# Kernel optimization log

Measured on AMD Instinct MI355X. Metric: run time of the kernel, lower is better.

Reference implementation:

```python
import jax, jax.numpy as jnp
import numpy as np

N = 4096            # total nodes in batched graph
B = 64              # number of graphs
NPG = 64            # nodes per graph (N = B * NPG)
HID = 64            # hidden_dim
INIT_EMB = 32       # init_emb_dim
POS = 32            # inp_dim (positional/structural feat)
KG = 100000         # num_nodes in KG embedding table
LAYER = 3           # num_gcn_layers


def setup_inputs() -> dict:
    key = jax.random.key(0)
    ks = jax.random.split(key, 10)
    # block-diagonal symmetric binary adjacency (batched graph, no self loops)
    gi = jnp.repeat(jnp.arange(B), NPG)                      # graph_indices [N]
    block = gi[:, None] == gi[None, :]
    u = jax.random.uniform(ks[0], (N, N)) < 0.1
    a = jnp.logical_and(jnp.logical_or(u, u.T), block)
    a = a.at[jnp.arange(N), jnp.arange(N)].set(False)
    adj = a.astype(jnp.float32)
    head_ids = jnp.arange(B) * NPG           # node with ndata['id']==1 per graph
    tail_ids = jnp.arange(B) * NPG + 1       # node with ndata['id']==2 per graph
    return {
        "adj": adj,
        "feat_node": jax.random.normal(ks[1], (N, POS), jnp.float32),
        "idx": jax.random.randint(ks[2], (N,), 0, KG),
        "head_ids": head_ids,
        "tail_ids": tail_ids,
        "graph_indices": gi,
        "transform": jax.random.normal(ks[3], (INIT_EMB + POS, HID), jnp.float32) * 0.05,
        "embed": jax.random.normal(ks[4], (KG, INIT_EMB), jnp.float32) * 0.05,
        "w1": jax.random.normal(ks[5], (HID, HID), jnp.float32) * 0.01,
        "b1": jnp.zeros((HID,), jnp.float32),
        "w2": jax.random.normal(ks[6], (HID, HID), jnp.float32) * 0.01,
        "b2": jnp.zeros((HID,), jnp.float32),
        "gamma1": jnp.ones((HID,), jnp.float32),
        "beta1": jnp.zeros((HID,), jnp.float32),
        "gamma2": jnp.ones((HID,), jnp.float32),
        "beta2": jnp.zeros((HID,), jnp.float32),
    }


def _att_light(query, nodefea, mask, gamma, beta):
    # Attention_light: correlation-weighted masked aggregation + LayerNorm
    cor = jnp.abs(jnp.sum(query * nodefea, axis=-1, keepdims=True))   # [N,1]
    wei = cor * nodefea                                               # [N,H]
    num_nei = jnp.sum(mask, axis=-1, keepdims=True)                   # [N,1]
    up = jax.nn.leaky_relu(mask @ wei, negative_slope=0.01)           # [N,H]
    x = up / (num_nei + 1e-8)
    mu = jnp.mean(x, axis=-1, keepdims=True)
    var = jnp.var(x, axis=-1, keepdims=True)                          # biased, as torch LN
    return gamma * (x - mu) / jnp.sqrt(var + 1e-5) + beta


def _agg(entity, neighbor, w, b):
    # Aggregator: relu((entity + neighbor) @ w + b)
    return jax.nn.relu((entity + neighbor) @ w + b)


def reference(adj, feat_node, idx, head_ids, tail_ids, graph_indices,
              transform, embed, w1, b1, w2, b2, gamma1, beta1, gamma2, beta2):
    n = adj.shape[0]
    diag = jnp.arange(n)
    # node features: cat(struct feat, KG embedding) @ transform
    init_feat = jnp.concatenate([feat_node, embed[idx]], axis=1)      # [N, INIT+POS]
    feat = init_feat @ transform                                      # [N, H]
    # per-node query features of the opposite center
    headQ = feat[head_ids][graph_indices]                             # all_c1_featQ [N,H]
    tailQ = feat[tail_ids][graph_indices]                             # all_c2_featQ [N,H]
    # adjacency powers A_0=I, A_k = binarize(A_{k-1} @ adj, diag=1)
    A = jnp.eye(n, dtype=adj.dtype)
    flat_h = [jnp.zeros((n,), adj.dtype).at[head_ids].add(1.0)]       # sum of A_0 head rows
    flat_t = [jnp.zeros((n,), adj.dtype).at[tail_ids].add(1.0)]
    for _ in range(LAYER - 1):
        M = A @ adj
        M = M.at[diag, diag].set(1.0)
        A = (M > 0).astype(adj.dtype)
        flat_h.append(jnp.sum(A[head_ids], axis=0))
        flat_t.append(jnp.sum(A[tail_ids], axis=0))
    # initial masked features (hop-0 indicator = head/tail node indicator)
    init_head = (flat_h[0] > 0).astype(feat.dtype)[:, None] * feat
    init_tail = (flat_t[0] > 0).astype(feat.dtype)[:, None] * feat
    all_feat_head = feat
    all_feat_tail = feat
    layer_all, layer_head, layer_tail = [feat], [init_head], [init_tail]
    for hop in range(LAYER - 1, -1, -1):
        f1 = flat_h[hop]                                              # [N], 0/1 per node
        f2 = flat_t[hop]
        mask1 = f1[:, None] * adj                                     # [N,N]
        mask2 = f2[:, None] * adj
        up1 = _att_light(tailQ, all_feat_head, mask1, gamma1, beta1)
        up2 = _att_light(headQ, all_feat_tail, mask2, gamma2, beta2)
        agg1 = _agg(f1[:, None] * feat, up1, w1, b1)
        agg2 = _agg(f2[:, None] * feat, up2, w2, b2)
        all_feat_head = jnp.where((f1 > 0)[:, None], agg1, all_feat_head)
        all_feat_tail = jnp.where((f2 > 0)[:, None], agg2, all_feat_tail)
        layer_all.append(all_feat_head + all_feat_tail)
        layer_head.append(all_feat_head)
        layer_tail.append(all_feat_tail)
    # cat along feature dim then view -> stack on new axis 1
    return jnp.stack(layer_all, axis=1)                               # [N, LAYER+1, H]
```

## Files before the change

kernel.cpp:

```cpp
#include <hip/hip_runtime.h>

#define LD 68
#define XP 72

typedef float f32x4 __attribute__((ext_vector_type(4)));
typedef short s16x8 __attribute__((ext_vector_type(8)));
typedef unsigned long long u64;

__device__ __forceinline__ unsigned short f2bf(float f) {
  union { float f; unsigned int u; } v; v.f = f;
  const unsigned int r = (v.u + 0x7fffu + ((v.u >> 16) & 1u)) >> 16;
  return (unsigned short)r;
}
__device__ __forceinline__ float bf2f(unsigned short h) {
  union { unsigned int u; float f; } v; v.u = ((unsigned int)h) << 16;
  return v.f;
}

__global__ __launch_bounds__(512) void lagat_kernel(
    const float* __restrict__ adj,
    const float* __restrict__ feat_node,
    const int* __restrict__ idx,
    const int* __restrict__ head_ids,
    const int* __restrict__ tail_ids,
    const float* __restrict__ transform,
    const float* __restrict__ embed,
    const float* __restrict__ w1, const float* __restrict__ b1,
    const float* __restrict__ w2, const float* __restrict__ b2,
    const float* __restrict__ gamma1, const float* __restrict__ beta1,
    const float* __restrict__ gamma2, const float* __restrict__ beta2,
    float* __restrict__ out)
{
  __shared__ __align__(16) unsigned short CSTs[2][64][XP];
  __shared__ __align__(16) float Sb[2][64][LD];
  __shared__ __align__(16) float featb[64][LD];
  __shared__ __align__(16) float Ab[64][LD];
  __shared__ __align__(16) float Ib[64][LD];
  __shared__ __align__(16) float Wb[2][4096];
  __shared__ __align__(16) float prm[2][3][64];
  __shared__ u64 adjbits[64];
  __shared__ u64 lev[2][3];
  __shared__ float degs[64];
  __shared__ float corr[2][64];

  const int g = blockIdx.x, tid = threadIdx.x, nb = g * 64;
  const int wv = tid >> 6, lane = tid & 63;
  const int ech = wv >> 2, eslab = (wv & 3) * 16;
  const int ln15 = lane & 15, lg = lane >> 4, lg4 = lg * 4;
  const int iNode = eslab + ln15;

  {
    const int r = tid >> 3, c8 = (tid & 7) * 8;
    const float4* asrc = (const float4*)&adj[(size_t)(nb + r) * 4096 + nb + c8];
    *(float4*)&Ab[r][c8]     = asrc[0];
    *(float4*)&Ab[r][c8 + 4] = asrc[1];
    if (c8 < 32) {
      const float4* fs = (const float4*)&feat_node[(size_t)(nb + r) * 32 + c8];
      *(float4*)&Ib[r][c8]     = fs[0];
      *(float4*)&Ib[r][c8 + 4] = fs[1];
    } else {
      const float4* es = (const float4*)&embed[(size_t)idx[nb + r] * 32 + (c8 - 32)];
      *(float4*)&Ib[r][c8]     = es[0];
      *(float4*)&Ib[r][c8 + 4] = es[1];
    }
  }
  {
    const int base = tid * 16;
    const float* src = (base < 4096) ? &w1[base] : &w2[base - 4096];
    float* dst = &Wb[0][0] + base;
#pragma unroll
    for (int u = 0; u < 4; ++u)
      *(float4*)&dst[u * 4] = *(const float4*)&src[u * 4];
  }
  if (tid < 384) {
    const int a = tid >> 6, h = tid & 63;
    const float* s6 = (a == 0) ? gamma1 : (a == 1) ? beta1 : (a == 2) ? b1
                    : (a == 3) ? gamma2 : (a == 4) ? beta2 : b2;
    prm[a / 3][a % 3][h] = s6[h];
  }
  __syncthreads();

  const int hl = head_ids[g] - nb, tl = tail_ids[g] - nb;

  {
#pragma unroll
    for (int rr = 0; rr < 8; ++rr) {
      const int row = wv * 8 + rr;
      const u64 b = __ballot(Ab[row][lane] != 0.0f);
      if (lane == 0) { adjbits[row] = b; degs[row] = (float)__popcll(b); }
    }
  }
  {
    const int c0g = (tid & 15) * 4, r0g = (tid >> 4) * 2;
    float a0c[4] = {}, a1c[4] = {};
    for (int k = 0; k < 64; ++k) {
      const float4 t4 = *(const float4*)&transform[(size_t)k * 64 + c0g];
      const float a0 = Ib[r0g][k], a1 = Ib[r0g + 1][k];
      a0c[0] = fmaf(a0, t4.x, a0c[0]); a0c[1] = fmaf(a0, t4.y, a0c[1]);
      a0c[2] = fmaf(a0, t4.z, a0c[2]); a0c[3] = fmaf(a0, t4.w, a0c[3]);
      a1c[0] = fmaf(a1, t4.x, a1c[0]); a1c[1] = fmaf(a1, t4.y, a1c[1]);
      a1c[2] = fmaf(a1, t4.z, a1c[2]); a1c[3] = fmaf(a1, t4.w, a1c[3]);
    }
    *(float4*)&featb[r0g][c0g]     = make_float4(a0c[0], a0c[1], a0c[2], a0c[3]);
    *(float4*)&featb[r0g + 1][c0g] = make_float4(a1c[0], a1c[1], a1c[2], a1c[3]);
  }
  s16x8 wfh[8], afr[2];
  {
    const float* Wl = Wb[ech];
#pragma unroll
    for (int ct = 0; ct < 4; ++ct)
#pragma unroll
      for (int ks = 0; ks < 2; ++ks) {
        s16x8 h;
#pragma unroll
        for (int j = 0; j < 8; ++j)
          h[j] = (short)f2bf(Wl[(ks * 32 + lg * 8 + j) * 64 + ct * 16 + ln15]);
        wfh[ct * 2 + ks] = h;
      }
#pragma unroll
    for (int ks = 0; ks < 2; ++ks) {
      const float4 a0 = *(const float4*)&Ab[iNode][ks * 32 + lg * 8];
      const float4 a1 = *(const float4*)&Ab[iNode][ks * 32 + lg * 8 + 4];
      s16x8 a;
      a[0] = (short)f2bf(a0.x); a[1] = (short)f2bf(a0.y);
      a[2] = (short)f2bf(a0.z); a[3] = (short)f2bf(a0.w);
      a[4] = (short)f2bf(a1.x); a[5] = (short)f2bf(a1.y);
      a[6] = (short)f2bf(a1.z); a[7] = (short)f2bf(a1.w);
      afr[ks] = a;
    }
  }
  __syncthreads();

  if (tid < 128) {
    const int c = wv;
    const int root = c ? tl : hl;
    const u64 l0 = 1ull << root;
    const u64 l1 = l0 | adjbits[root];
    u64 cand = ((l1 >> lane) & 1ull) ? adjbits[lane] : 0ull;
#pragma unroll
    for (int m = 1; m < 64; m <<= 1) cand |= __shfl_xor(cand, m, 64);
    if (lane == 0) { lev[c][0] = l0; lev[c][1] = l1; lev[c][2] = l0 | cand; }
  }
  {
    const int ch2 = tid >> 8, t = tid & 255;
    const int j = t >> 2, q = t & 3;
    const int qr = ch2 ? hl : tl;
    float s = 0.f;
#pragma unroll
    for (int u = 0; u < 4; ++u) {
      const float4 q4 = *(const float4*)&featb[qr][q * 16 + 4 * u];
      const float4 f4 = *(const float4*)&featb[j][q * 16 + 4 * u];
      s = fmaf(q4.x, f4.x, s); s = fmaf(q4.y, f4.y, s);
      s = fmaf(q4.z, f4.z, s); s = fmaf(q4.w, f4.w, s);
    }
    s += __shfl_xor(s, 1);
    s += __shfl_xor(s, 2);
    if (q == 0) corr[ch2][j] = fabsf(s);
  }
  {
    const int r = tid >> 3, c8 = (tid & 7) * 8;
#pragma unroll
    for (int u = 0; u < 2; ++u) {
      const float4 v = *(const float4*)&featb[r][c8 + 4 * u];
      *(float4*)&Sb[0][r][c8 + 4 * u] = v;
      *(float4*)&Sb[1][r][c8 + 4 * u] = v;
      *(float4*)&out[(size_t)(nb + r) * 256 + c8 + 4 * u] = v;
    }
  }
  const float dnv = 1.f / (degs[iNode] + 1e-8f);
  f32x4 ft4[4];
#pragma unroll
  for (int ct = 0; ct < 4; ++ct) {
    const int ebase = ((ct >> 1) << 5) + lg * 8 + ((ct & 1) << 2);
    ft4[ct] = *(const f32x4*)&featb[iNode][ebase];
  }
  __syncthreads();

  {
    const int ch2 = tid >> 8, t = tid & 255;
    const int c = t >> 2, j0 = (t & 3) * 16;
    const int rho = ((c >> 5) & 1) * 32 + ((c >> 2) & 1) * 16 +
                    ((c >> 4) & 1) * 8 + ((c >> 3) & 1) * 4 + (c & 3);
#pragma unroll
    for (int half = 0; half < 2; ++half) {
      s16x8 hh;
#pragma unroll
      for (int m = 0; m < 8; ++m) {
        const int j = j0 + half * 8 + m;
        hh[m] = (short)f2bf(corr[ch2][j] * featb[j][c]);
      }
      *(s16x8*)&CSTs[ch2][rho][j0 + half * 8] = hh;
    }
  }
  __syncthreads();

  const int r8 = tid >> 3, cc8 = (tid & 7) * 8;
  const int qrowE = ech ? hl : tl;

  u64 levCh[3];
#pragma unroll
  for (int k = 0; k < 3; ++k) levCh[k] = lev[ech][k];
  f32x4 qe4[4], bias4[4];
#pragma unroll
  for (int ct = 0; ct < 4; ++ct) {
    qe4[ct] = *(const f32x4*)&featb[qrowE][ct * 16 + lg4];
    bias4[ct] = *(const f32x4*)&prm[ech][2][ct * 16 + lg4];
  }

  for (int hop = 2; hop >= 0; --hop) {
    if (hop != 2) {
      const int L = 2 - hop;
#pragma unroll
      for (int u = 0; u < 2; ++u) {
        const float4 a = *(const float4*)&Sb[0][r8][cc8 + 4 * u];
        const float4 b = *(const float4*)&Sb[1][r8][cc8 + 4 * u];
        *(float4*)&out[(size_t)(nb + r8) * 256 + (size_t)L * 64 + cc8 + 4 * u] =
            make_float4(a.x + b.x, a.y + b.y, a.z + b.z, a.w + b.w);
      }
    }

    f32x4 accB[4] = {{0,0,0,0},{0,0,0,0},{0,0,0,0},{0,0,0,0}};
#pragma unroll
    for (int ct = 0; ct < 4; ++ct)
#pragma unroll
      for (int ks = 0; ks < 2; ++ks) {
        const s16x8 ah = *(const s16x8*)&CSTs[ech][ct * 16 + ln15][ks * 32 + lg * 8];
        accB[ct] = __builtin_amdgcn_mfma_f32_16x16x32_bf16(ah, afr[ks], accB[ct], 0, 0, 0);
      }
    const float fB = (float)((levCh[hop] >> iNode) & 1ull);
    float x[4][4];
    {
      float smm = 0.f, s2m = 0.f;
#pragma unroll
      for (int ct = 0; ct < 4; ++ct)
#pragma unroll
        for (int r = 0; r < 4; ++r) {
          float z = accB[ct][r];
          z = (z > 0.f) ? z : 0.01f * z;
          z *= dnv;
          x[ct][r] = z; smm += z; s2m = fmaf(z, z, s2m);
        }
      smm += __shfl_xor(smm, 16); smm += __shfl_xor(smm, 32);
      s2m += __shfl_xor(s2m, 16); s2m += __shfl_xor(s2m, 32);
      const float mu = smm * 0.015625f;
      const float var = fmaxf(s2m * 0.015625f - mu * mu, 0.f);
      const float rstd = rsqrtf(var + 1e-5f);
#pragma unroll
      for (int ct = 0; ct < 4; ++ct) {
        const int ebase = ((ct >> 1) << 5) + lg * 8 + ((ct & 1) << 2);
        const f32x4 ga4 = *(const f32x4*)&prm[ech][0][ebase];
        const f32x4 be4 = *(const f32x4*)&prm[ech][1][ebase];
#pragma unroll
        for (int r = 0; r < 4; ++r)
          x[ct][r] = fmaf(fB, ft4[ct][r], ga4[r] * (x[ct][r] - mu) * rstd + be4[r]);
      }
    }
    s16x8 xh2[2], xl2[2];
#pragma unroll
    for (int ks = 0; ks < 2; ++ks) {
      s16x8 hh, ll;
#pragma unroll
      for (int j = 0; j < 8; ++j) {
        const float xv = x[2 * ks + (j >> 2)][j & 3];
        const unsigned short h = f2bf(xv);
        hh[j] = (short)h;
        ll[j] = (short)f2bf(xv - bf2f(h));
      }
      xh2[ks] = hh; xl2[ks] = ll;
    }
    f32x4 accE[4];
#pragma unroll
    for (int ct = 0; ct < 4; ++ct) {
      accE[ct] = bias4[ct];
#pragma unroll
      for (int ks = 0; ks < 2; ++ks) {
        accE[ct] = __builtin_amdgcn_mfma_f32_16x16x32_bf16(wfh[ct*2+ks], xh2[ks], accE[ct], 0, 0, 0);
        accE[ct] = __builtin_amdgcn_mfma_f32_16x16x32_bf16(wfh[ct*2+ks], xl2[ks], accE[ct], 0, 0, 0);
      }
    }
    float s[4][4], v = 0.f;
#pragma unroll
    for (int ct = 0; ct < 4; ++ct)
#pragma unroll
      for (int r = 0; r < 4; ++r) {
        const float sv = fmaxf(accE[ct][r], 0.f);
        s[ct][r] = sv;
        v = fmaf(qe4[ct][r], sv, v);
      }
    v += __shfl_xor(v, 16); v += __shfl_xor(v, 32);
    const float vc = fabsf(v);
    const float fE = (float)((levCh[hop] >> iNode) & 1ull);

    __syncthreads();

    if (fE != 0.f) {
#pragma unroll
      for (int ct = 0; ct < 4; ++ct) {
        *(float4*)&Sb[ech][iNode][ct * 16 + lg4] =
            make_float4(s[ct][0], s[ct][1], s[ct][2], s[ct][3]);
        if (hop) {
          const int rbase = ((ct >> 1) << 5) + ((lg & 1) << 4) +
                            ((ct & 1) << 3) + ((lg >> 1) << 2);
#pragma unroll
          for (int r = 0; r < 4; ++r)
            CSTs[ech][rbase + r][iNode] = f2bf(vc * s[ct][r]);
        }
      }
    }
    __syncthreads();
  }

  {
#pragma unroll
    for (int u = 0; u < 2; ++u) {
      const float4 a = *(const float4*)&Sb[0][r8][cc8 + 4 * u];
      const float4 b = *(const float4*)&Sb[1][r8][cc8 + 4 * u];
      *(float4*)&out[(size_t)(nb + r8) * 256 + 192 + cc8 + 4 * u] =
          make_float4(a.x + b.x, a.y + b.y, a.z + b.z, a.w + b.w);
    }
  }
}

extern "C" void kernel_launch(void* const* d_in, const int* in_sizes, int n_in,
                              void* d_out, int out_size, void* d_ws, size_t ws_size,
                              hipStream_t stream) {
  const float* adj       = (const float*)d_in[0];
  const float* feat_node = (const float*)d_in[1];
  const int*   idx       = (const int*)d_in[2];
  const int*   head_ids  = (const int*)d_in[3];
  const int*   tail_ids  = (const int*)d_in[4];
  const float* transform = (const float*)d_in[6];
  const float* embed     = (const float*)d_in[7];
  const float* w1v    = (const float*)d_in[8];
  const float* b1v    = (const float*)d_in[9];
  const float* w2v    = (const float*)d_in[10];
  const float* b2v    = (const float*)d_in[11];
  const float* gamma1 = (const float*)d_in[12];
  const float* beta1  = (const float*)d_in[13];
  const float* gamma2 = (const float*)d_in[14];
  const float* beta2  = (const float*)d_in[15];

  lagat_kernel<<<64, 512, 0, stream>>>(adj, feat_node, idx, head_ids, tail_ids,
      transform, embed, w1v, b1v, w2v, b2v, gamma1, beta1, gamma2, beta2,
      (float*)d_out);
}
```

Baseline: 21.28 us.

## Ballot adjacency straight from global and compute feature transform with MFMA

The adjacency block is no longer staged in shared memory. Each row is ballotted directly from global into bitmasks, and the bf16 A fragments are built from those bits. The transform matrix is staged in LDS, and the input-feature projection now runs on MFMA in half the waves, using split hi/lo bf16 operands for the input to keep accuracy, instead of scalar FMAs against global memory. This removes one __syncthreads and the Ab buffer, and moves degree and BFS-level computation together. The trade-offs are some precision loss, because the transform weights are rounded to single bf16, and idle waves during the projection.

After: 19.49 us. 8.4% less time.

```diff
diff --git a/kernel.cpp b/kernel.cpp
--- a/kernel.cpp
+++ b/kernel.cpp
@@ -34,9 +34,9 @@
   __shared__ __align__(16) unsigned short CSTs[2][64][XP];
   __shared__ __align__(16) float Sb[2][64][LD];
   __shared__ __align__(16) float featb[64][LD];
-  __shared__ __align__(16) float Ab[64][LD];
   __shared__ __align__(16) float Ib[64][LD];
   __shared__ __align__(16) float Wb[2][4096];
+  __shared__ __align__(16) float Tb[4096];
   __shared__ __align__(16) float prm[2][3][64];
   __shared__ u64 adjbits[64];
   __shared__ u64 lev[2][3];
@@ -50,10 +50,15 @@
   const int iNode = eslab + ln15;
 
   {
+#pragma unroll
+    for (int rr = 0; rr < 8; ++rr) {
+      const int row = wv * 8 + rr;
+      const u64 b = __ballot(adj[(size_t)(nb + row) * 4096 + nb + lane] != 0.0f);
+      if (lane == 0) adjbits[row] = b;
+    }
+  }
+  {
     const int r = tid >> 3, c8 = (tid & 7) * 8;
-    const float4* asrc = (const float4*)&adj[(size_t)(nb + r) * 4096 + nb + c8];
-    *(float4*)&Ab[r][c8]     = asrc[0];
-    *(float4*)&Ab[r][c8 + 4] = asrc[1];
     if (c8 < 32) {
       const float4* fs = (const float4*)&feat_node[(size_t)(nb + r) * 32 + c8];
       *(float4*)&Ib[r][c8]     = fs[0];
@@ -72,6 +77,11 @@
     for (int u = 0; u < 4; ++u)
       *(float4*)&dst[u * 4] = *(const float4*)&src[u * 4];
   }
+  {
+    const int tb = tid * 8;
+    *(float4*)&Tb[tb]     = *(const float4*)&transform[tb];
+    *(float4*)&Tb[tb + 4] = *(const float4*)&transform[tb + 4];
+  }
   if (tid < 384) {
     const int a = tid >> 6, h = tid & 63;
     const float* s6 = (a == 0) ? gamma1 : (a == 1) ? beta1 : (a == 2) ? b1
@@ -82,57 +92,10 @@
 
   const int hl = head_ids[g] - nb, tl = tail_ids[g] - nb;
 
-  {
-#pragma unroll
-    for (int rr = 0; rr < 8; ++rr) {
-      const int row = wv * 8 + rr;
-      const u64 b = __ballot(Ab[row][lane] != 0.0f);
-      if (lane == 0) { adjbits[row] = b; degs[row] = (float)__popcll(b); }
-    }
-  }
-  {
-    const int c0g = (tid & 15) * 4, r0g = (tid >> 4) * 2;
-    float a0c[4] = {}, a1c[4] = {};
-    for (int k = 0; k < 64; ++k) {
-      const float4 t4 = *(const float4*)&transform[(size_t)k * 64 + c0g];
-      const float a0 = Ib[r0g][k], a1 = Ib[r0g + 1][k];
-      a0c[0] = fmaf(a0, t4.x, a0c[0]); a0c[1] = fmaf(a0, t4.y, a0c[1]);
-      a0c[2] = fmaf(a0, t4.z, a0c[2]); a0c[3] = fmaf(a0, t4.w, a0c[3]);
-      a1c[0] = fmaf(a1, t4.x, a1c[0]); a1c[1] = fmaf(a1, t4.y, a1c[1]);
-      a1c[2] = fmaf(a1, t4.z, a1c[2]); a1c[3] = fmaf(a1, t4.w, a1c[3]);
-    }
-    *(float4*)&featb[r0g][c0g]     = make_float4(a0c[0], a0c[1], a0c[2], a0c[3]);
-    *(float4*)&featb[r0g + 1][c0g] = make_float4(a1c[0], a1c[1], a1c[2], a1c[3]);
-  }
-  s16x8 wfh[8], afr[2];
-  {
-    const float* Wl = Wb[ech];
-#pragma unroll
-    for (int ct = 0; ct < 4; ++ct)
-#pragma unroll
-      for (int ks = 0; ks < 2; ++ks) {
-        s16x8 h;
-#pragma unroll
-        for (int j = 0; j < 8; ++j)
-          h[j] = (short)f2bf(Wl[(ks * 32 + lg * 8 + j) * 64 + ct * 16 + ln15]);
-        wfh[ct * 2 + ks] = h;
-      }
-#pragma unroll
-    for (int ks = 0; ks < 2; ++ks) {
-      const float4 a0 = *(const float4*)&Ab[iNode][ks * 32 + lg * 8];
-      const float4 a1 = *(const float4*)&Ab[iNode][ks * 32 + lg * 8 + 4];
-      s16x8 a;
-      a[0] = (short)f2bf(a0.x); a[1] = (short)f2bf(a0.y);
-      a[2] = (short)f2bf(a0.z); a[3] = (short)f2bf(a0.w);
-      a[4] = (short)f2bf(a1.x); a[5] = (short)f2bf(a1.y);
-      a[6] = (short)f2bf(a1.z); a[7] = (short)f2bf(a1.w);
-      afr[ks] = a;
-    }
-  }
-  __syncthreads();
-
-  if (tid < 128) {
-    const int c = wv;
+  if (tid < 64) {
+    degs[tid] = (float)__popcll(adjbits[tid]);
+  } else if (tid < 192) {
+    const int c = (tid >> 6) - 1;
     const int root = c ? tl : hl;
     const u64 l0 = 1ull << root;
     const u64 l1 = l0 | adjbits[root];
@@ -141,6 +104,64 @@
     for (int m = 1; m < 64; m <<= 1) cand |= __shfl_xor(cand, m, 64);
     if (lane == 0) { lev[c][0] = l0; lev[c][1] = l1; lev[c][2] = l0 | cand; }
   }
+  s16x8 wfh[8], afr[2];
+  {
+    const float* Wl = Wb[ech];
+#pragma unroll
+    for (int ct = 0; ct < 4; ++ct)
+#pragma unroll
+      for (int ks = 0; ks < 2; ++ks) {
+        s16x8 h;
+#pragma unroll
+        for (int j = 0; j < 8; ++j)
+          h[j] = (short)f2bf(Wl[(ks * 32 + lg * 8 + j) * 64 + ct * 16 + ln15]);
+        wfh[ct * 2 + ks] = h;
+      }
+    const u64 abits = adjbits[iNode];
+#pragma unroll
+    for (int ks = 0; ks < 2; ++ks) {
+      s16x8 a;
+#pragma unroll
+      for (int j = 0; j < 8; ++j)
+        a[j] = (short)(((abits >> (ks * 32 + lg * 8 + j)) & 1ull) ? 0x3F80 : 0);
+      afr[ks] = a;
+    }
+  }
+  if (ech == 0) {
+    s16x8 ihf[2], ilf[2];
+#pragma unroll
+    for (int ks = 0; ks < 2; ++ks) {
+      const float4 i0 = *(const float4*)&Ib[iNode][ks * 32 + lg * 8];
+      const float4 i1 = *(const float4*)&Ib[iNode][ks * 32 + lg * 8 + 4];
+      const float iv[8] = {i0.x, i0.y, i0.z, i0.w, i1.x, i1.y, i1.z, i1.w};
+      s16x8 hh, ll;
+#pragma unroll
+      for (int j = 0; j < 8; ++j) {
+        const unsigned short h = f2bf(iv[j]);
+        hh[j] = (short)h;
+        ll[j] = (short)f2bf(iv[j] - bf2f(h));
+      }
+      ihf[ks] = hh; ilf[ks] = ll;
+    }
+    f32x4 facc[4] = {{0,0,0,0},{0,0,0,0},{0,0,0,0},{0,0,0,0}};
+#pragma unroll
+    for (int ct = 0; ct < 4; ++ct)
+#pragma unroll
+      for (int ks = 0; ks < 2; ++ks) {
+        s16x8 th;
+#pragma unroll
+        for (int j = 0; j < 8; ++j)
+          th[j] = (short)f2bf(Tb[(ks * 32 + lg * 8 + j) * 64 + ct * 16 + ln15]);
+        facc[ct] = __builtin_amdgcn_mfma_f32_16x16x32_bf16(th, ihf[ks], facc[ct], 0, 0, 0);
+        facc[ct] = __builtin_amdgcn_mfma_f32_16x16x32_bf16(th, ilf[ks], facc[ct], 0, 0, 0);
+      }
+#pragma unroll
+    for (int ct = 0; ct < 4; ++ct)
+      *(float4*)&featb[iNode][ct * 16 + lg4] =
+          make_float4(facc[ct][0], facc[ct][1], facc[ct][2], facc[ct][3]);
+  }
+  __syncthreads();
+
   {
     const int ch2 = tid >> 8, t = tid & 255;
     const int j = t >> 2, q = t & 3;
```
